# Performance work log

Hardware: AMD Instinct MI355X
Metric: run time of the kernel (lower is better)

## Reference

```python
import jax, jax.numpy as jnp
import numpy as np

HEAD_DIM = 32
KSIZE = 3
SCALE = HEAD_DIM ** (-0.5)  # self.scale = head_dim ** -0.5 with head_dim=32


def setup_inputs() -> dict:
    key = jax.random.key(0)
    kq, kk, kv = jax.random.split(key, 3)
    shape = (4, 128, 128, 128)  # (B, d, H, W)
    return {
        "q": jax.random.normal(kq, shape, dtype=jnp.float32),
        "k": jax.random.normal(kk, shape, dtype=jnp.float32),
        "v": jax.random.normal(kv, shape, dtype=jnp.float32),
    }


def _unfold3(x):
    # nn.Unfold(kernel_size=3, dilation=1, padding=1, stride=1):
    # [B, d, H, W] -> [B, d, 9, H, W], kernel positions in row-major (ki, kj)
    B, d, H, W = x.shape
    xp = jnp.pad(x, ((0, 0), (0, 0), (1, 1), (1, 1)))
    return jnp.stack(
        [xp[:, :, i:i + H, j:j + W] for i in range(KSIZE) for j in range(KSIZE)],
        axis=2,
    )


def reference(q, k, v):
    B, d, H, W = q.shape
    h = d // HEAD_DIM  # number of heads
    n = H * W
    # q: [B, h, head_dim, n]
    qh = q.reshape(B, h, HEAD_DIM, n)
    # k patches: [B, h, head_dim, 9, n]
    kp = _unfold3(k).reshape(B, h, HEAD_DIM, KSIZE * KSIZE, n)
    # attn: [B, h, n, 9] = (q . k_neighbor) * scale, softmax over the 9 neighbors
    attn = jnp.einsum('bhcn,bhckn->bhnk', qh, kp) * SCALE
    attn = jax.nn.softmax(attn, axis=-1)
    # v patches: [B, h, head_dim, 9, n]
    vp = _unfold3(v).reshape(B, h, HEAD_DIM, KSIZE * KSIZE, n)
    # out: [B, n, h, head_dim] -> [B, H, W, d] (head-major channel layout, as in torch)
    out = jnp.einsum('bhnk,bhckn->bnhc', attn, vp).reshape(B, H, W, d)
    return jax.nn.relu(out)
```

## Files before the change

kernel.cpp:

```cpp
#include <hip/hip_runtime.h>

#define HW 128
#define PLANE (HW * HW)
#define SCALE 0.17677669529663687f
#define FENCE() asm volatile("" ::: "memory")

__global__ __launch_bounds__(512, 2) void natt3x3_kernel(
    const float* __restrict__ q,
    const float* __restrict__ k,
    const float* __restrict__ v,
    float* __restrict__ out) {
  const int tid  = threadIdx.x;
  const int lane = tid & 63;
  const int w    = tid >> 6;
  const int h2   = lane & 1;
  const int s    = lane >> 1;
  const int x0   = s << 2;
  const int bid  = blockIdx.x;
  const int img   = ((bid & 7) << 1) | ((bid >> 3) & 1);
  const int ytile = bid >> 4;
  const int head  = img & 3;
  const int b     = img >> 2;
  const int y     = (ytile << 3) | w;

  const size_t cbase = (size_t)(b * 128 + head * 32 + h2 * 4) * PLANE;
  const int yx = y * HW + x0;

  int yrow[3];
#pragma unroll
  for (int dy = 0; dy < 3; ++dy) {
    int yy = y + dy - 1; yy = yy < 0 ? 0 : (yy > HW - 1 ? HW - 1 : yy);
    yrow[dy] = yy * HW;
  }

  float l[4][9];
#pragma unroll
  for (int i = 0; i < 4; ++i)
#pragma unroll
    for (int j = 0; j < 9; ++j) l[i][j] = 0.f;

  float acc[4][16];
#pragma unroll
  for (int i = 0; i < 4; ++i)
#pragma unroll
    for (int c = 0; c < 16; ++c) acc[i][c] = 0.f;

  float4 qv4[3][4];
  float4 rv[3][3][4];

#define LQK(B, G) do {                                                       \
    const size_t cb = cbase + (size_t)((G) * 8) * PLANE;                     \
    const float* qg = q + cb + yx;                                           \
    const float* kg = k + cb;                                                \
    _Pragma("unroll")                                                        \
    for (int c = 0; c < 4; ++c)                                              \
      qv4[B][c] = *reinterpret_cast<const float4*>(qg + (size_t)c * PLANE);  \
    _Pragma("unroll")                                                        \
    for (int c = 0; c < 4; ++c)                                              \
      _Pragma("unroll")                                                      \
      for (int dy = 0; dy < 3; ++dy)                                         \
        rv[B][dy][c] = *reinterpret_cast<const float4*>(                     \
            kg + (size_t)c * PLANE + yrow[dy] + x0);                         \
  } while (0)

#define LPV(B, G) do {                                                       \
    const float* vg = v + cbase + (size_t)((G) * 8) * PLANE;                 \
    _Pragma("unroll")                                                        \
    for (int c = 0; c < 4; ++c)                                              \
      _Pragma("unroll")                                                      \
      for (int dy = 0; dy < 3; ++dy)                                         \
        rv[B][dy][c] = *reinterpret_cast<const float4*>(                     \
            vg + (size_t)c * PLANE + yrow[dy] + x0);                         \
  } while (0)

#define CQK(B) do {                                                          \
    _Pragma("unroll")                                                        \
    for (int c = 0; c < 4; ++c) {                                            \
      const float qa[4] = {qv4[B][c].x * SCALE, qv4[B][c].y * SCALE,         \
                           qv4[B][c].z * SCALE, qv4[B][c].w * SCALE};        \
      _Pragma("unroll")                                                      \
      for (int dy = 0; dy < 3; ++dy) {                                       \
        float4 kq = rv[B][dy][c];                                            \
        float n0 = __shfl_up(kq.w, 2);                                       \
        float n5 = __shfl_down(kq.x, 2);                                     \
        const float n[6] = {n0, kq.x, kq.y, kq.z, kq.w, n5};                 \
        _Pragma("unroll")                                                    \
        for (int i = 0; i < 4; ++i)                                          \
          _Pragma("unroll")                                                  \
          for (int j = 0; j < 3; ++j)                                        \
            l[i][dy * 3 + j] += qa[i] * n[i + j];                            \
      }                                                                      \
    }                                                                        \
  } while (0)

#define CPV(B, G) do {                                                       \
    _Pragma("unroll")                                                        \
    for (int c = 0; c < 4; ++c)                                              \
      _Pragma("unroll")                                                      \
      for (int dy = 0; dy < 3; ++dy) {                                       \
        float4 vq = rv[B][dy][c];                                            \
        float n0 = __shfl_up(vq.w, 2);                                       \
        float n5 = __shfl_down(vq.x, 2);                                     \
        const float n[6] = {n0, vq.x, vq.y, vq.z, vq.w, n5};                 \
        _Pragma("unroll")                                                    \
        for (int i = 0; i < 4; ++i)                                          \
          _Pragma("unroll")                                                  \
          for (int j = 0; j < 3; ++j)                                        \
            acc[i][(G) * 4 + c] += l[i][dy * 3 + j] * n[i + j];              \
      }                                                                      \
  } while (0)

  LQK(0, 0); FENCE();
  LQK(1, 1); FENCE();
  LQK(2, 2); FENCE();
  CQK(0);    FENCE();
  LQK(0, 3); FENCE();
  CQK(1);    FENCE();
  LPV(1, 0); FENCE();
  CQK(2);    FENCE();
  LPV(2, 1); FENCE();
  CQK(0);    FENCE();
  LPV(0, 2); FENCE();

#pragma unroll
  for (int i = 0; i < 4; ++i)
#pragma unroll
    for (int j = 0; j < 9; ++j) l[i][j] += __shfl_xor(l[i][j], 1);

#pragma unroll
  for (int i = 0; i < 4; ++i) {
    const int xp = x0 + i;
    float mk[9];
#pragma unroll
    for (int dy = 0; dy < 3; ++dy)
#pragma unroll
      for (int dx = 0; dx < 3; ++dx) {
        bool ok = ((unsigned)(y + dy - 1) < (unsigned)HW) &&
                  ((unsigned)(xp + dx - 1) < (unsigned)HW);
        mk[dy * 3 + dx] = ok ? 1.f : 0.f;
      }
    float m = -1e30f;
#pragma unroll
    for (int j = 0; j < 9; ++j) {
      float t = l[i][j] * mk[j];
      l[i][j] = t;
      m = fmaxf(m, t);
    }
    float sum = 0.f;
#pragma unroll
    for (int j = 0; j < 9; ++j) {
      float e = __expf(l[i][j] - m);
      l[i][j] = e;
      sum += e;
    }
    float inv = 1.f / sum;
#pragma unroll
    for (int j = 0; j < 9; ++j) l[i][j] *= inv * mk[j];
  }
  FENCE();

  CPV(1, 0); FENCE();
  LPV(1, 3); FENCE();
  CPV(2, 1); FENCE();
  CPV(0, 2); FENCE();
  CPV(1, 3);

  const size_t obase = ((size_t)(b * PLANE + y * HW)) * 128 + head * 32 + h2 * 4;
#pragma unroll
  for (int i = 0; i < 4; ++i) {
    float* op = out + obase + (size_t)(x0 + i) * 128;
#pragma unroll
    for (int g = 0; g < 4; ++g) {
      float4 o;
      o.x = fmaxf(acc[i][g * 4 + 0], 0.f);
      o.y = fmaxf(acc[i][g * 4 + 1], 0.f);
      o.z = fmaxf(acc[i][g * 4 + 2], 0.f);
      o.w = fmaxf(acc[i][g * 4 + 3], 0.f);
      *reinterpret_cast<float4*>(op + g * 8) = o;
    }
  }

#undef LQK
#undef LPV
#undef CQK
#undef CPV
}

extern "C" void kernel_launch(void* const* d_in, const int* in_sizes, int n_in,
                              void* d_out, int out_size, void* d_ws, size_t ws_size,
                              hipStream_t stream) {
  const float* q = (const float*)d_in[0];
  const float* k = (const float*)d_in[1];
  const float* v = (const float*)d_in[2];
  float* out = (float*)d_out;
  natt3x3_kernel<<<256, 512, 0, stream>>>(q, k, v, out);
}
```

Measured before the change: 27.83 us.

## Stage K/V halo rows in LDS via direct global-to-LDS DMA with triple buffering

Instead of each wave loading its three K/V rows (overlapping neighbours' rows) straight into registers, the block cooperatively DMAs a 10-row halo tile per channel group into LDS with global_load_lds, triple-buffered, and waves read their rows from shared memory. This removes the threefold redundant global/L2 reads of K and V rows across waves and frees the large register staging arrays. In exchange it adds 120 KB of LDS per block, block barriers, and hand-tuned vmcnt waits whose counts must exactly match outstanding loads, which is fragile and may limit occupancy.

```diff
diff --git a/kernel.cpp b/kernel.cpp
--- a/kernel.cpp
+++ b/kernel.cpp
@@ -1,15 +1,26 @@
 #include <hip/hip_runtime.h>
+#include <stdint.h>
 
 #define HW 128
 #define PLANE (HW * HW)
 #define SCALE 0.17677669529663687f
 #define FENCE() asm volatile("" ::: "memory")
+#define VMW(N) asm volatile("s_waitcnt vmcnt(" #N ")" ::: "memory")
+#define BAR() __builtin_amdgcn_s_barrier()
+
+__device__ __forceinline__ void dma16(const float* g, float* l) {
+  __builtin_amdgcn_global_load_lds(
+      (const __attribute__((address_space(1))) void*)g,
+      (__attribute__((address_space(3))) void*)l, 16, 0, 0);
+}
 
 __global__ __launch_bounds__(512, 2) void natt3x3_kernel(
     const float* __restrict__ q,
     const float* __restrict__ k,
     const float* __restrict__ v,
     float* __restrict__ out) {
+  __shared__ __align__(16) float smem[3 * 10240];
+
   const int tid  = threadIdx.x;
   const int lane = tid & 63;
   const int w    = tid >> 6;
@@ -21,112 +32,114 @@
   const int ytile = bid >> 4;
   const int head  = img & 3;
   const int b     = img >> 2;
-  const int y     = (ytile << 3) | w;
-
-  const size_t cbase = (size_t)(b * 128 + head * 32 + h2 * 4) * PLANE;
+  const int y0    = ytile << 3;
+  const int y     = y0 + w;
+
+  const size_t ibase = (size_t)(b * 128 + head * 32) * PLANE;
+  const size_t cbase = ibase + (size_t)(h2 * 4) * PLANE;
   const int yx = y * HW + x0;
 
-  int yrow[3];
-#pragma unroll
-  for (int dy = 0; dy < 3; ++dy) {
-    int yy = y + dy - 1; yy = yy < 0 ? 0 : (yy > HW - 1 ? HW - 1 : yy);
-    yrow[dy] = yy * HW;
+  const int hi  = lane >> 5;
+  const int spx = (lane & 31) << 2;
+  int srow[5];
+#pragma unroll
+  for (int j = 0; j < 5; ++j) {
+    int rg = y0 - 1 + 2 * j + hi;
+    rg = rg < 0 ? 0 : (rg > HW - 1 ? HW - 1 : rg);
+    srow[j] = rg * HW + spx;
   }
+  float* const dwave = smem + w * 1280;
 
   float l[4][9];
 #pragma unroll
   for (int i = 0; i < 4; ++i)
 #pragma unroll
     for (int j = 0; j < 9; ++j) l[i][j] = 0.f;
-
   float acc[4][16];
 #pragma unroll
   for (int i = 0; i < 4; ++i)
 #pragma unroll
     for (int c = 0; c < 16; ++c) acc[i][c] = 0.f;
-
-  float4 qv4[3][4];
-  float4 rv[3][3][4];
-
-#define LQK(B, G) do {                                                       \
-    const size_t cb = cbase + (size_t)((G) * 8) * PLANE;                     \
-    const float* qg = q + cb + yx;                                           \
-    const float* kg = k + cb;                                                \
-    _Pragma("unroll")                                                        \
-    for (int c = 0; c < 4; ++c)                                              \
-      qv4[B][c] = *reinterpret_cast<const float4*>(qg + (size_t)c * PLANE);  \
-    _Pragma("unroll")                                                        \
-    for (int c = 0; c < 4; ++c)                                              \
-      _Pragma("unroll")                                                      \
-      for (int dy = 0; dy < 3; ++dy)                                         \
-        rv[B][dy][c] = *reinterpret_cast<const float4*>(                     \
-            kg + (size_t)c * PLANE + yrow[dy] + x0);                         \
-  } while (0)
-
-#define LPV(B, G) do {                                                       \
-    const float* vg = v + cbase + (size_t)((G) * 8) * PLANE;                 \
-    _Pragma("unroll")                                                        \
-    for (int c = 0; c < 4; ++c)                                              \
-      _Pragma("unroll")                                                      \
-      for (int dy = 0; dy < 3; ++dy)                                         \
-        rv[B][dy][c] = *reinterpret_cast<const float4*>(                     \
-            vg + (size_t)c * PLANE + yrow[dy] + x0);                         \
-  } while (0)
-
-#define CQK(B) do {                                                          \
-    _Pragma("unroll")                                                        \
-    for (int c = 0; c < 4; ++c) {                                            \
-      const float qa[4] = {qv4[B][c].x * SCALE, qv4[B][c].y * SCALE,         \
-                           qv4[B][c].z * SCALE, qv4[B][c].w * SCALE};        \
-      _Pragma("unroll")                                                      \
-      for (int dy = 0; dy < 3; ++dy) {                                       \
-        float4 kq = rv[B][dy][c];                                            \
-        float n0 = __shfl_up(kq.w, 2);                                       \
-        float n5 = __shfl_down(kq.x, 2);                                     \
-        const float n[6] = {n0, kq.x, kq.y, kq.z, kq.w, n5};                 \
-        _Pragma("unroll")                                                    \
-        for (int i = 0; i < 4; ++i)                                          \
-          _Pragma("unroll")                                                  \
-          for (int j = 0; j < 3; ++j)                                        \
-            l[i][dy * 3 + j] += qa[i] * n[i + j];                            \
-      }                                                                      \
-    }                                                                        \
-  } while (0)
-
-#define CPV(B, G) do {                                                       \
-    _Pragma("unroll")                                                        \
-    for (int c = 0; c < 4; ++c)                                              \
-      _Pragma("unroll")                                                      \
-      for (int dy = 0; dy < 3; ++dy) {                                       \
-        float4 vq = rv[B][dy][c];                                            \
-        float n0 = __shfl_up(vq.w, 2);                                       \
-        float n5 = __shfl_down(vq.x, 2);                                     \
-        const float n[6] = {n0, vq.x, vq.y, vq.z, vq.w, n5};                 \
-        _Pragma("unroll")                                                    \
-        for (int i = 0; i < 4; ++i)                                          \
-          _Pragma("unroll")                                                  \
-          for (int j = 0; j < 3; ++j)                                        \
-            acc[i][(G) * 4 + c] += l[i][dy * 3 + j] * n[i + j];              \
-      }                                                                      \
-  } while (0)
-
-  LQK(0, 0); FENCE();
-  LQK(1, 1); FENCE();
-  LQK(2, 2); FENCE();
-  CQK(0);    FENCE();
-  LQK(0, 3); FENCE();
-  CQK(1);    FENCE();
-  LPV(1, 0); FENCE();
-  CQK(2);    FENCE();
-  LPV(2, 1); FENCE();
-  CQK(0);    FENCE();
-  LPV(0, 2); FENCE();
+  float4 qA[4], qB[4];
+
+#define DMA(BUF, PTR, G) do {                                                 \
+    const float* sb = (PTR) + ibase + (size_t)((G) * 8 + w) * PLANE;          \
+    float* db = dwave + (BUF) * 10240;                                        \
+    _Pragma("unroll")                                                         \
+    for (int j = 0; j < 5; ++j) dma16(sb + srow[j], db + j * 256);            \
+  } while (0)
+
+#define LQ(QW, G) do {                                                        \
+    const float* qg = q + cbase + (size_t)((G) * 8) * PLANE + yx;             \
+    _Pragma("unroll")                                                         \
+    for (int c = 0; c < 4; ++c)                                               \
+      QW[c] = *reinterpret_cast<const float4*>(qg + (size_t)c * PLANE);       \
+  } while (0)
+
+#define SKV(BUF, C, DY)                                                       \
+  (*reinterpret_cast<const float4*>(                                          \
+      smem + (BUF) * 10240 + (h2 * 4 + (C)) * 1280 + (w + (DY)) * 128 + x0))
+
+#define CQK(BUF, QW) do {                                                     \
+    _Pragma("unroll")                                                         \
+    for (int c = 0; c < 4; ++c) {                                             \
+      const float qa[4] = {QW[c].x * SCALE, QW[c].y * SCALE,                  \
+                           QW[c].z * SCALE, QW[c].w * SCALE};                 \
+      _Pragma("unroll")                                                       \
+      for (int dy = 0; dy < 3; ++dy) {                                        \
+        float4 kq = SKV(BUF, c, dy);                                          \
+        float n0 = __shfl_up(kq.w, 2);                                        \
+        float n5 = __shfl_down(kq.x, 2);                                      \
+        const float n[6] = {n0, kq.x, kq.y, kq.z, kq.w, n5};                  \
+        _Pragma("unroll")                                                     \
+        for (int i = 0; i < 4; ++i)                                           \
+          _Pragma("unroll")                                                   \
+          for (int j = 0; j < 3; ++j)                                         \
+            l[i][dy * 3 + j] += qa[i] * n[i + j];                             \
+      }                                                                       \
+    }                                                                         \
+  } while (0)
+
+#define CPV(BUF, G) do {                                                      \
+    _Pragma("unroll")                                                         \
+    for (int c = 0; c < 4; ++c)                                               \
+      _Pragma("unroll")                                                       \
+      for (int dy = 0; dy < 3; ++dy) {                                        \
+        float4 vq = SKV(BUF, c, dy);                                          \
+        float n0 = __shfl_up(vq.w, 2);                                        \
+        float n5 = __shfl_down(vq.x, 2);                                      \
+        const float n[6] = {n0, vq.x, vq.y, vq.z, vq.w, n5};                  \
+        _Pragma("unroll")                                                     \
+        for (int i = 0; i < 4; ++i)                                           \
+          _Pragma("unroll")                                                   \
+          for (int j = 0; j < 3; ++j)                                         \
+            acc[i][(G) * 4 + c] += l[i][dy * 3 + j] * n[i + j];               \
+      }                                                                       \
+  } while (0)
+
+  LQ(qA, 0);     FENCE();
+  DMA(0, k, 0);  FENCE();
+  DMA(1, k, 1);  FENCE();
+  LQ(qB, 1);     FENCE();
+  DMA(2, k, 2);  FENCE();
+  VMW(14); BAR(); FENCE();
+  CQK(0, qA);    FENCE(); BAR(); FENCE();
+  LQ(qA, 2);     FENCE();
+  DMA(0, k, 3);  FENCE();
+  VMW(18); BAR(); FENCE();
+  CQK(1, qB);    FENCE(); BAR(); FENCE();
+  LQ(qB, 3);     FENCE();
+  DMA(1, v, 0);  FENCE();
+  VMW(18); BAR(); FENCE();
+  CQK(2, qA);    FENCE(); BAR(); FENCE();
+  DMA(2, v, 1);  FENCE();
+  VMW(14); BAR(); FENCE();
+  CQK(0, qB);    FENCE();
 
 #pragma unroll
   for (int i = 0; i < 4; ++i)
 #pragma unroll
     for (int j = 0; j < 9; ++j) l[i][j] += __shfl_xor(l[i][j], 1);
-
 #pragma unroll
   for (int i = 0; i < 4; ++i) {
     const int xp = x0 + i;
@@ -157,12 +170,16 @@
 #pragma unroll
     for (int j = 0; j < 9; ++j) l[i][j] *= inv * mk[j];
   }
-  FENCE();
-
-  CPV(1, 0); FENCE();
-  LPV(1, 3); FENCE();
-  CPV(2, 1); FENCE();
-  CPV(0, 2); FENCE();
+  FENCE(); BAR(); FENCE();
+  DMA(0, v, 2);  FENCE();
+  VMW(10); BAR(); FENCE();
+  CPV(1, 0);     FENCE(); BAR(); FENCE();
+  DMA(1, v, 3);  FENCE();
+  VMW(10); BAR(); FENCE();
+  CPV(2, 1);     FENCE(); BAR(); FENCE();
+  VMW(5); BAR(); FENCE();
+  CPV(0, 2);     FENCE(); BAR(); FENCE();
+  VMW(0); BAR(); FENCE();
   CPV(1, 3);
 
   const size_t obase = ((size_t)(b * PLANE + y * HW)) * 128 + head * 32 + h2 * 4;
@@ -180,8 +197,9 @@
     }
   }
 
-#undef LQK
-#undef LPV
+#undef DMA
+#undef LQ
+#undef SKV
 #undef CQK
 #undef CPV
 }
```

Result: slower. 31.83 us (+14.4%).
